# Performance work log

Hardware: AMD Instinct MI355X
Metric: run time of the kernel (lower is better)

The kernel has to match this reference:

```python
import jax, jax.numpy as jnp
import numpy as np

B, L, D_MODEL = 2, 2048, 1024
N_HEADS, D_K = 16, 64  # d_v == d_k (required by the output*q epilogue)


def setup_inputs() -> dict:
    key = jax.random.key(0)
    ks = jax.random.split(key, 8)
    # xavier_normal std for [d_model, d_k] fan: sqrt(2/(d_model+d_k))
    std = float(np.sqrt(2.0 / (D_MODEL + D_K)))
    std_p = float(np.sqrt(1.0 / (N_HEADS * D_K)))  # nn.Linear default ~ U(-1/sqrt(fan_in),..); normal approx ok for a baseline
    return {
        "q": jax.random.normal(ks[0], (B, L, D_MODEL), jnp.float32),
        "k": jax.random.normal(ks[1], (B, L, D_MODEL), jnp.float32),
        "v": jax.random.normal(ks[2], (B, L, D_MODEL), jnp.float32),
        "w_qs": jax.random.normal(ks[3], (N_HEADS, D_MODEL, D_K), jnp.float32) * std,
        "w_ks": jax.random.normal(ks[4], (N_HEADS, D_MODEL, D_K), jnp.float32) * std,
        "w_vs": jax.random.normal(ks[5], (N_HEADS, D_MODEL, D_K), jnp.float32) * std,
        "w_proj": jax.random.normal(ks[6], (D_MODEL, N_HEADS * D_K), jnp.float32) * std_p,
        "b_proj": jnp.zeros((D_MODEL,), jnp.float32),
    }


def reference(q, k, v, w_qs, w_ks, w_vs, w_proj, b_proj):
    # Per-head projections: [h, B, L, d_k]
    qh = jnp.einsum("bld,hdk->hblk", q, w_qs)
    kh = jnp.einsum("bld,hdk->hblk", k, w_ks)
    vh = jnp.einsum("bld,hdk->hblk", v, w_vs)
    # UNscaled attention (no 1/sqrt(d_k)), dropout is identity at eval
    attn = jax.nn.softmax(jnp.einsum("hblk,hbmk->hblm", qh, kh), axis=-1)
    # attn @ V with elementwise *q epilogue
    out = jnp.einsum("hblm,hbmk->hblk", attn, vh) * qh
    # torch.cat(torch.split(outputs, mb_size, 0), -1): heads concat on last dim
    out = out.transpose(1, 2, 0, 3).reshape(q.shape[0], q.shape[1], -1)  # [B, L, h*d_k]
    return out @ w_proj.T + b_proj
```

## Files before the change

kernel.cpp:

```cpp
#include <hip/hip_runtime.h>

#define B_ 2
#define L_ 2048
#define DM 1024
#define H_ 16
#define DK 64
#define ROWS (B_*L_)
#define BK 32
#define LDT 40

typedef _Float16 f16x8 __attribute__((ext_vector_type(8)));
typedef float    f32x4 __attribute__((ext_vector_type(4)));
typedef unsigned short us8 __attribute__((ext_vector_type(8)));
typedef unsigned short us4v __attribute__((ext_vector_type(4)));

__device__ __forceinline__ unsigned short f2h(float f) {
    _Float16 h = (_Float16)f;
    return __builtin_bit_cast(unsigned short, h);
}
__device__ __forceinline__ float h2f(unsigned short u) {
    return (float)__builtin_bit_cast(_Float16, u);
}
__device__ __forceinline__ f16x8 ld8h(const unsigned short* p) {
    return *reinterpret_cast<const f16x8*>(p);
}
__device__ __forceinline__ us8 cvt_us8(float4 a, float4 b) {
    us8 u;
    u[0] = f2h(a.x); u[1] = f2h(a.y); u[2] = f2h(a.z); u[3] = f2h(a.w);
    u[4] = f2h(b.x); u[5] = f2h(b.y); u[6] = f2h(b.z); u[7] = f2h(b.w);
    return u;
}

#define MFMA(a, b, c) __builtin_amdgcn_mfma_f32_16x16x32_f16((a), (b), (c), 0, 0, 0)

#define AS1 __attribute__((address_space(1)))
#define AS3 __attribute__((address_space(3)))
__device__ __forceinline__ void glds16(const void* g, void* l) {
    __builtin_amdgcn_global_load_lds((const AS1 unsigned int*)g,
                                     (AS3 unsigned int*)l, 16, 0, 0);
}

__global__ __launch_bounds__(256) void kcvt(
    const float* __restrict__ src, unsigned short* __restrict__ dst)
{
    size_t i = ((size_t)blockIdx.x * 256 + threadIdx.x) * 8;
    const float4* s4 = (const float4*)(src + i);
    *(us8*)(dst + i) = cvt_us8(s4[0], s4[1]);
}

__global__ __launch_bounds__(256) void kcvt3(
    const float* __restrict__ q, const float* __restrict__ k,
    const float* __restrict__ v, unsigned short* __restrict__ dst)
{
    int bx = blockIdx.x;
    int which = bx >> 11, rem = bx & 2047;
    const float* src = (which == 0) ? q : (which == 1) ? k : v;
    size_t i = ((size_t)rem * 256 + threadIdx.x) * 8;
    const float4* s4 = (const float4*)(src + i);
    *(us8*)(dst + (size_t)which * ROWS * DM + i) = cvt_us8(s4[0], s4[1]);
}

__global__ __launch_bounds__(256) void k0_transpose_w(
    const float* __restrict__ wq,
    const float* __restrict__ wk,
    const float* __restrict__ wv,
    unsigned short* __restrict__ wt)
{
    __shared__ unsigned short tile[64][65];
    int bx = blockIdx.x;
    int which = bx / (H_ * 16);
    int rem   = bx % (H_ * 16);
    int h  = rem >> 4;
    int db = (rem & 15) * 64;
    const float* src = (which == 0) ? wq : (which == 1) ? wk : wv;
    float scale = (which == 1) ? 1.44269504f : 1.0f;

    int t = threadIdx.x;
    int r = t >> 2;
    int c = (t & 3) * 16;
    const float4* sp = (const float4*)(src + ((size_t)(h * DM + db + r)) * DK + c);
    #pragma unroll
    for (int i4 = 0; i4 < 4; i4++) {
        float4 f = sp[i4];
        tile[r][c + i4 * 4 + 0] = f2h(f.x * scale);
        tile[r][c + i4 * 4 + 1] = f2h(f.y * scale);
        tile[r][c + i4 * 4 + 2] = f2h(f.z * scale);
        tile[r][c + i4 * 4 + 3] = f2h(f.w * scale);
    }
    __syncthreads();

    int n   = t >> 2;
    int d16 = (t & 3) * 16;
    __align__(16) unsigned short ov[16];
    #pragma unroll
    for (int i = 0; i < 16; i++) ov[i] = tile[d16 + i][n];
    size_t off = (((size_t)which * H_ + h) * DK + n) * DM + db + d16;
    *(us8*)(wt + off)     = *(us8*)&ov[0];
    *(us8*)(wt + off + 8) = *(us8*)&ov[8];
}

__global__ __launch_bounds__(256) void k1_proj_fp16(
    const unsigned short* __restrict__ qkvh,
    const unsigned short* __restrict__ wt,
    unsigned short* __restrict__ qh,
    unsigned short* __restrict__ kh,
    unsigned short* __restrict__ vt)
{
    __shared__ __align__(16) unsigned short sA[128 * BK];
    __shared__ __align__(16) unsigned short sB[128 * BK];

    int bx = blockIdx.x;
    int which = bx >> 8;
    int rem   = bx & 255;
    int mbase = (rem >> 3) * 128;
    int nbase = (rem & 7) * 128;

    const unsigned short* Ag = qkvh + (size_t)which * ROWS * DM;
    const unsigned short* Bg = wt + (size_t)which * DM * DM;

    int t = threadIdx.x;
    int wave = t >> 6, lane = t & 63, quad = lane >> 4, l16 = lane & 15;
    int wm = (wave >> 1) * 64, wn = (wave & 1) * 64;

    const unsigned short* gA0 = Ag + (size_t)(mbase + (t >> 2)) * DM + (t & 3) * 8;
    const unsigned short* gA1 = gA0 + (size_t)64 * DM;
    const unsigned short* gB0 = Bg + (size_t)(nbase + (t >> 2)) * DM + (t & 3) * 8;
    const unsigned short* gB1 = gB0 + (size_t)64 * DM;
    unsigned short* lA0 = &sA[(size_t)t * 8];
    unsigned short* lA1 = &sA[(size_t)(256 + t) * 8];
    unsigned short* lB0 = &sB[(size_t)t * 8];
    unsigned short* lB1 = &sB[(size_t)(256 + t) * 8];

    f32x4 acc[4][4];
    #pragma unroll
    for (int mi = 0; mi < 4; mi++)
        #pragma unroll
        for (int ni = 0; ni < 4; ni++) acc[mi][ni] = (f32x4)0.0f;

    for (int step = 0; step < 32; step++) {
        if (step) __syncthreads();
        glds16(gA0, lA0); glds16(gA1, lA1);
        glds16(gB0, lB0); glds16(gB1, lB1);
        gA0 += BK; gA1 += BK; gB0 += BK; gB1 += BK;
        __syncthreads();

        f16x8 aF[4], bF[4];
        #pragma unroll
        for (int mi = 0; mi < 4; mi++)
            aF[mi] = *(const f16x8*)&sA[(wm + mi * 16 + l16) * BK + quad * 8];
        #pragma unroll
        for (int ni = 0; ni < 4; ni++)
            bF[ni] = *(const f16x8*)&sB[(wn + ni * 16 + l16) * BK + quad * 8];
        __builtin_amdgcn_s_setprio(1);
        #pragma unroll
        for (int mi = 0; mi < 4; mi++)
            #pragma unroll
            for (int ni = 0; ni < 4; ni++)
                acc[mi][ni] = MFMA(aF[mi], bF[ni], acc[mi][ni]);
        __builtin_amdgcn_s_setprio(0);
    }

    int h = (nbase >> 6) + (wave & 1);
    if (which < 2) {
        unsigned short* OUT = ((which == 0) ? qh : kh) + (size_t)h * ROWS * DK;
        #pragma unroll
        for (int mi = 0; mi < 4; mi++)
            #pragma unroll
            for (int ni = 0; ni < 4; ni++)
                #pragma unroll
                for (int r = 0; r < 4; r++) {
                    int row = mbase + wm + mi * 16 + quad * 4 + r;
                    OUT[(size_t)row * DK + ni * 16 + l16] = f2h(acc[mi][ni][r]);
                }
    } else {
        unsigned short* OUT = vt + (size_t)h * DK * ROWS;
        #pragma unroll
        for (int mi = 0; mi < 4; mi++)
            #pragma unroll
            for (int ni = 0; ni < 4; ni++) {
                int dk   = ni * 16 + l16;
                int rowb = mbase + wm + mi * 16 + quad * 4;
                us4v pk;
                pk[0] = f2h(acc[mi][ni][0]); pk[1] = f2h(acc[mi][ni][1]);
                pk[2] = f2h(acc[mi][ni][2]); pk[3] = f2h(acc[mi][ni][3]);
                *(us4v*)(OUT + (size_t)dk * ROWS + rowb) = pk;
            }
    }
}

__global__ __launch_bounds__(256) void k1_proj_qkv(
    const float* __restrict__ q,
    const float* __restrict__ k,
    const float* __restrict__ v,
    const unsigned short* __restrict__ wt,
    unsigned short* __restrict__ qh,
    unsigned short* __restrict__ kh,
    unsigned short* __restrict__ vt)
{
    __shared__ __align__(16) unsigned short sA[128 * LDT];
    __shared__ __align__(16) unsigned short sB[128 * LDT];

    int bx = blockIdx.x;
    int which = bx >> 8;
    int rem   = bx & 255;
    int mbase = (rem >> 3) * 128;
    int nbase = (rem & 7) * 128;

    const float* Ag = (which == 0) ? q : (which == 1) ? k : v;
    const unsigned short* Bg = wt + (size_t)which * DM * DM;

    int t = threadIdx.x;
    int wave = t >> 6, lane = t & 63, quad = lane >> 4, l16 = lane & 15;
    int wm = (wave >> 1) * 64, wn = (wave & 1) * 64;

    int ar0 = t >> 2,         ac0 = t & 3;
    int ar1 = (256 + t) >> 2, ac1 = t & 3;
    const float* pA0 = Ag + (size_t)(mbase + ar0) * DM + ac0 * 8;
    const float* pA1 = Ag + (size_t)(mbase + ar1) * DM + ac1 * 8;
    const unsigned short* pB0 = Bg + (size_t)(nbase + ar0) * DM + ac0 * 8;
    const unsigned short* pB1 = Bg + (size_t)(nbase + ar1) * DM + ac1 * 8;
    unsigned short* wA0 = &sA[ar0 * LDT + ac0 * 8];
    unsigned short* wA1 = &sA[ar1 * LDT + ac1 * 8];
    unsigned short* wB0 = &sB[ar0 * LDT + ac0 * 8];
    unsigned short* wB1 = &sB[ar1 * LDT + ac1 * 8];

    f32x4 acc[4][4];
    #pragma unroll
    for (int mi = 0; mi < 4; mi++)
        #pragma unroll
        for (int ni = 0; ni < 4; ni++) acc[mi][ni] = (f32x4)0.0f;

    float4 rA0a = *(const float4*)pA0, rA0b = *(const float4*)(pA0 + 4);
    float4 rA1a = *(const float4*)pA1, rA1b = *(const float4*)(pA1 + 4);
    us8 rB0 = *(const us8*)pB0, rB1 = *(const us8*)pB1;

    for (int step = 0; step < 32; step++) {
        if (step) __syncthreads();
        *(us8*)wA0 = cvt_us8(rA0a, rA0b);
        *(us8*)wA1 = cvt_us8(rA1a, rA1b);
        *(us8*)wB0 = rB0; *(us8*)wB1 = rB1;
        __syncthreads();
        if (step < 31) {
            pA0 += BK; pA1 += BK; pB0 += BK; pB1 += BK;
            rA0a = *(const float4*)pA0; rA0b = *(const float4*)(pA0 + 4);
            rA1a = *(const float4*)pA1; rA1b = *(const float4*)(pA1 + 4);
            rB0 = *(const us8*)pB0; rB1 = *(const us8*)pB1;
        }
        f16x8 aF[4], bF[4];
        #pragma unroll
        for (int mi = 0; mi < 4; mi++)
            aF[mi] = *(const f16x8*)&sA[(wm + mi * 16 + l16) * LDT + quad * 8];
        #pragma unroll
        for (int ni = 0; ni < 4; ni++)
            bF[ni] = *(const f16x8*)&sB[(wn + ni * 16 + l16) * LDT + quad * 8];
        #pragma unroll
        for (int mi = 0; mi < 4; mi++)
            #pragma unroll
            for (int ni = 0; ni < 4; ni++)
                acc[mi][ni] = MFMA(aF[mi], bF[ni], acc[mi][ni]);
    }

    int h = (nbase >> 6) + (wave & 1);
    if (which < 2) {
        unsigned short* OUT = ((which == 0) ? qh : kh) + (size_t)h * ROWS * DK;
        #pragma unroll
        for (int mi = 0; mi < 4; mi++)
            #pragma unroll
            for (int ni = 0; ni < 4; ni++)
                #pragma unroll
                for (int r = 0; r < 4; r++) {
                    int row = mbase + wm + mi * 16 + quad * 4 + r;
                    OUT[(size_t)row * DK + ni * 16 + l16] = f2h(acc[mi][ni][r]);
                }
    } else {
        unsigned short* OUT = vt + (size_t)h * DK * ROWS;
        #pragma unroll
        for (int mi = 0; mi < 4; mi++)
            #pragma unroll
            for (int ni = 0; ni < 4; ni++) {
                int dk   = ni * 16 + l16;
                int rowb = mbase + wm + mi * 16 + quad * 4;
                us4v pk;
                pk[0] = f2h(acc[mi][ni][0]); pk[1] = f2h(acc[mi][ni][1]);
                pk[2] = f2h(acc[mi][ni][2]); pk[3] = f2h(acc[mi][ni][3]);
                *(us4v*)(OUT + (size_t)dk * ROWS + rowb) = pk;
            }
    }
}

__global__ __launch_bounds__(256) void k2_attn(
    const unsigned short* __restrict__ qh,
    const unsigned short* __restrict__ kh,
    const unsigned short* __restrict__ vt,
    unsigned short* __restrict__ x2)
{
    __shared__ __align__(16) unsigned short ktile[2][64][64];
    __shared__ __align__(16) unsigned short vtile[2][64][64];
    __shared__ __align__(16) unsigned short pld[4][16][64];

    int bx = blockIdx.x;
    int xcd = bx & 7;
    int loc = bx >> 3;
    int hb  = xcd * 4 + (loc >> 5);
    int qt  = loc & 31;
    int h = hb >> 1, b = hb & 1;
    int qbase = qt * 64;

    const unsigned short* qhp = qh + ((size_t)h * ROWS + b * L_) * DK;
    const unsigned short* khp = kh + ((size_t)h * ROWS + b * L_) * DK;
    const unsigned short* vtp = vt + (size_t)h * DK * ROWS + b * L_;

    int wave = threadIdx.x >> 6, lane = threadIdx.x & 63;
    int quad = lane >> 4, l16 = lane & 15;
    int t = threadIdx.x;
    int g8 = (l16 & 7) * 8;

    int c0 = t,       key0 = c0 >> 3, ss0 = ((c0 & 7) ^ (key0 & 7)) * 8;
    int c1 = 256 + t, key1 = c1 >> 3, ss1 = ((c1 & 7) ^ (key1 & 7)) * 8;
    const unsigned short* kg0 = khp + (size_t)key0 * DK + ss0;
    const unsigned short* kg1 = khp + (size_t)key1 * DK + ss1;
    const unsigned short* vg0 = vtp + (size_t)key0 * ROWS + ss0;
    const unsigned short* vg1 = vtp + (size_t)key1 * ROWS + ss1;
    unsigned short* kl0[2] = { &ktile[0][0][0] + c0 * 8, &ktile[1][0][0] + c0 * 8 };
    unsigned short* kl1[2] = { &ktile[0][0][0] + c1 * 8, &ktile[1][0][0] + c1 * 8 };
    unsigned short* vl0[2] = { &vtile[0][0][0] + c0 * 8, &vtile[1][0][0] + c0 * 8 };
    unsigned short* vl1[2] = { &vtile[0][0][0] + c1 * 8, &vtile[1][0][0] + c1 * 8 };

    glds16(kg0, kl0[0]); glds16(kg1, kl1[0]);
    glds16(vg0, vl0[0]); glds16(vg1, vl1[0]);

    int qrow = qbase + wave * 16 + l16;
    f16x8 qb0 = ld8h(qhp + (size_t)qrow * DK + quad * 8);
    f16x8 qb1 = ld8h(qhp + (size_t)qrow * DK + 32 + quad * 8);

    float m_i = -1e30f, l_i = 0.0f;
    f32x4 o[4];
    #pragma unroll
    for (int nt = 0; nt < 4; nt++) o[nt] = (f32x4)0.0f;

    __syncthreads();

    int cur = 0;
    for (int kt = 0; kt < 32; kt++) {
        if (kt < 31) {
            size_t ko = (size_t)(kt + 1) * 64 * DK;
            size_t vo = (size_t)(kt + 1) * 64;
            int nb = cur ^ 1;
            glds16(kg0 + ko, kl0[nb]); glds16(kg1 + ko, kl1[nb]);
            glds16(vg0 + vo, vl0[nb]); glds16(vg1 + vo, vl1[nb]);
        }

        f32x4 s[4];
        #pragma unroll
        for (int nt = 0; nt < 4; nt++) s[nt] = (f32x4)0.0f;
        __builtin_amdgcn_s_setprio(1);
        #pragma unroll
        for (int nt = 0; nt < 4; nt++) {
            const unsigned short* kr = &ktile[cur][nt * 16 + l16][0];
            f16x8 ka0 = *(const f16x8*)(kr + ((quad * 8) ^ g8));
            f16x8 ka1 = *(const f16x8*)(kr + ((32 + quad * 8) ^ g8));
            s[nt] = MFMA(ka0, qb0, s[nt]);
            s[nt] = MFMA(ka1, qb1, s[nt]);
        }
        __builtin_amdgcn_s_setprio(0);

        float pm[4];
        #pragma unroll
        for (int nt = 0; nt < 4; nt++) {
            float a = fmaxf(s[nt][0], s[nt][1]);
            float c2 = fmaxf(s[nt][2], s[nt][3]);
            pm[nt] = fmaxf(a, c2);
        }
        float mx = fmaxf(fmaxf(pm[0], pm[1]), fmaxf(pm[2], pm[3]));
        mx = fmaxf(mx, __shfl_xor(mx, 16));
        mx = fmaxf(mx, __shfl_xor(mx, 32));

        if (!__all(mx - m_i <= 11.0f)) {
            float mnew  = fmaxf(m_i, mx);
            float alpha = __builtin_amdgcn_exp2f(m_i - mnew);
            l_i *= alpha;
            #pragma unroll
            for (int r = 0; r < 4; r++) {
                float av = __shfl(alpha, quad * 4 + r);
                #pragma unroll
                for (int nt = 0; nt < 4; nt++) o[nt][r] *= av;
            }
            m_i = mnew;
        }

        float ps[4];
        #pragma unroll
        for (int nt = 0; nt < 4; nt++) {
            float e0 = __builtin_amdgcn_exp2f(s[nt][0] - m_i);
            float e1 = __builtin_amdgcn_exp2f(s[nt][1] - m_i);
            float e2 = __builtin_amdgcn_exp2f(s[nt][2] - m_i);
            float e3 = __builtin_amdgcn_exp2f(s[nt][3] - m_i);
            s[nt][0] = e0; s[nt][1] = e1; s[nt][2] = e2; s[nt][3] = e3;
            ps[nt] = (e0 + e1) + (e2 + e3);
        }
        float rs = (ps[0] + ps[1]) + (ps[2] + ps[3]);
        rs += __shfl_xor(rs, 16);
        rs += __shfl_xor(rs, 32);
        l_i += rs;

        #pragma unroll
        for (int nt = 0; nt < 4; nt++) {
            us4v pk;
            pk[0] = f2h(s[nt][0]); pk[1] = f2h(s[nt][1]);
            pk[2] = f2h(s[nt][2]); pk[3] = f2h(s[nt][3]);
            *(us4v*)&pld[wave][l16][(nt * 16 + quad * 4) ^ g8] = pk;
        }

        __builtin_amdgcn_s_setprio(1);
        #pragma unroll
        for (int kk = 0; kk < 2; kk++) {
            f16x8 pa = *(const f16x8*)&pld[wave][l16][(kk * 32 + quad * 8) ^ g8];
            #pragma unroll
            for (int nt = 0; nt < 4; nt++) {
                const unsigned short* vr = &vtile[cur][nt * 16 + l16][0];
                f16x8 vb = *(const f16x8*)(vr + ((kk * 32 + quad * 8) ^ g8));
                o[nt] = MFMA(pa, vb, o[nt]);
            }
        }
        __builtin_amdgcn_s_setprio(0);

        __syncthreads();
        cur ^= 1;
    }

    float linv = 1.0f / l_i;
    #pragma unroll
    for (int r = 0; r < 4; r++) {
        float lv = __shfl(linv, quad * 4 + r);
        int row = qbase + wave * 16 + quad * 4 + r;
        #pragma unroll
        for (int nt = 0; nt < 4; nt++) {
            int col = nt * 16 + l16;
            float qv = h2f(qhp[(size_t)row * DK + col]);
            float val = o[nt][r] * lv * qv;
            x2[((size_t)b * L_ + row) * DM + h * DK + col] = f2h(val);
        }
    }
}

__global__ __launch_bounds__(256) void k3_out_proj(
    const unsigned short* __restrict__ x2,
    const unsigned short* __restrict__ wph,
    const float* __restrict__ bias,
    float* __restrict__ out)
{
    __shared__ __align__(16) unsigned short sA[128 * BK];
    __shared__ __align__(16) unsigned short sB[128 * BK];

    int bx = blockIdx.x;
    int mbase = (bx >> 3) * 128;
    int nbase = (bx & 7) * 128;

    int t = threadIdx.x;
    int wave = t >> 6, lane = t & 63, quad = lane >> 4, l16 = lane & 15;
    int wm = (wave >> 1) * 64, wn = (wave & 1) * 64;

    const unsigned short* gA0 = x2 + (size_t)(mbase + (t >> 2)) * DM + (t & 3) * 8;
    const unsigned short* gA1 = gA0 + (size_t)64 * DM;
    const unsigned short* gB0 = wph + (size_t)(nbase + (t >> 2)) * DM + (t & 3) * 8;
    const unsigned short* gB1 = gB0 + (size_t)64 * DM;
    unsigned short* lA0 = &sA[(size_t)t * 8];
    unsigned short* lA1 = &sA[(size_t)(256 + t) * 8];
    unsigned short* lB0 = &sB[(size_t)t * 8];
    unsigned short* lB1 = &sB[(size_t)(256 + t) * 8];

    f32x4 acc[4][4];
    #pragma unroll
    for (int mi = 0; mi < 4; mi++)
        #pragma unroll
        for (int ni = 0; ni < 4; ni++) acc[mi][ni] = (f32x4)0.0f;

    for (int step = 0; step < 32; step++) {
        if (step) __syncthreads();
        glds16(gA0, lA0); glds16(gA1, lA1);
        glds16(gB0, lB0); glds16(gB1, lB1);
        gA0 += BK; gA1 += BK; gB0 += BK; gB1 += BK;
        __syncthreads();

        f16x8 aF[4], bF[4];
        #pragma unroll
        for (int mi = 0; mi < 4; mi++)
            aF[mi] = *(const f16x8*)&sA[(wm + mi * 16 + l16) * BK + quad * 8];
        #pragma unroll
        for (int ni = 0; ni < 4; ni++)
            bF[ni] = *(const f16x8*)&sB[(wn + ni * 16 + l16) * BK + quad * 8];
        __builtin_amdgcn_s_setprio(1);
        #pragma unroll
        for (int mi = 0; mi < 4; mi++)
            #pragma unroll
            for (int ni = 0; ni < 4; ni++)
                acc[mi][ni] = MFMA(aF[mi], bF[ni], acc[mi][ni]);
        __builtin_amdgcn_s_setprio(0);
    }

    float bv[4];
    #pragma unroll
    for (int ni = 0; ni < 4; ni++) bv[ni] = bias[nbase + wn + ni * 16 + l16];

    #pragma unroll
    for (int mi = 0; mi < 4; mi++)
        #pragma unroll
        for (int ni = 0; ni < 4; ni++)
            #pragma unroll
            for (int r = 0; r < 4; r++) {
                int row = mbase + wm + mi * 16 + quad * 4 + r;
                int col = nbase + wn + ni * 16 + l16;
                out[(size_t)row * DM + col] = acc[mi][ni][r] + bv[ni];
            }
}

extern "C" void kernel_launch(void* const* d_in, const int* in_sizes, int n_in,
                              void* d_out, int out_size, void* d_ws, size_t ws_size,
                              hipStream_t stream)
{
    const float* q     = (const float*)d_in[0];
    const float* k     = (const float*)d_in[1];
    const float* v     = (const float*)d_in[2];
    const float* wqs   = (const float*)d_in[3];
    const float* wks   = (const float*)d_in[4];
    const float* wvs   = (const float*)d_in[5];
    const float* wproj = (const float*)d_in[6];
    const float* bproj = (const float*)d_in[7];
    float* out = (float*)d_out;

    char* ws = (char*)d_ws;
    #define MB (size_t)(1024 * 1024)
    unsigned short* wt   = (unsigned short*)(ws);
    unsigned short* wph  = (unsigned short*)(ws + 6  * MB);
    unsigned short* qh   = (unsigned short*)(ws + 8  * MB);
    unsigned short* kh   = (unsigned short*)(ws + 16 * MB);
    unsigned short* vt   = (unsigned short*)(ws + 24 * MB);
    unsigned short* x2   = (unsigned short*)(ws + 32 * MB);
    unsigned short* qkvh = (unsigned short*)(ws + 32 * MB);

    kcvt<<<dim3((DM * DM) / (256 * 8)), dim3(256), 0, stream>>>(wproj, wph);
    k0_transpose_w<<<dim3(3 * H_ * 16), dim3(256), 0, stream>>>(wqs, wks, wvs, wt);

    if (ws_size >= 56 * MB) {
        kcvt3<<<dim3(3 * 2048), dim3(256), 0, stream>>>(q, k, v, qkvh);
        k1_proj_fp16<<<dim3(3 * 32 * 8), dim3(256), 0, stream>>>(qkvh, wt, qh, kh, vt);
    } else {
        k1_proj_qkv<<<dim3(3 * 32 * 8), dim3(256), 0, stream>>>(q, k, v, wt, qh, kh, vt);
    }
    k2_attn<<<dim3(H_ * B_ * 32), dim3(256), 0, stream>>>(qh, kh, vt, x2);
    k3_out_proj<<<dim3(32 * 8), dim3(256), 0, stream>>>(x2, wph, bproj, out);
}
```

Baseline: 249.1 us.

## Software-pipeline QK^T of next tile with softmax and PV of current tile

```diff
diff --git a/kernel.cpp b/kernel.cpp
--- a/kernel.cpp
+++ b/kernel.cpp
@@ -326,7 +326,13 @@
     unsigned short* vl0[2] = { &vtile[0][0][0] + c0 * 8, &vtile[1][0][0] + c0 * 8 };
     unsigned short* vl1[2] = { &vtile[0][0][0] + c1 * 8, &vtile[1][0][0] + c1 * 8 };
 
+    const unsigned short* kgp0 = kg0 + (size_t)2 * 64 * DK;
+    const unsigned short* kgp1 = kg1 + (size_t)2 * 64 * DK;
+    const unsigned short* vgp0 = vg0 + 64;
+    const unsigned short* vgp1 = vg1 + 64;
+
     glds16(kg0, kl0[0]); glds16(kg1, kl1[0]);
+    glds16(kg0 + (size_t)64 * DK, kl0[1]); glds16(kg1 + (size_t)64 * DK, kl1[1]);
     glds16(vg0, vl0[0]); glds16(vg1, vl1[0]);
 
     int qrow = qbase + wave * 16 + l16;
@@ -338,95 +344,113 @@
     #pragma unroll
     for (int nt = 0; nt < 4; nt++) o[nt] = (f32x4)0.0f;
 
+    f32x4 s0[4], s1[4];
+
     __syncthreads();
 
-    int cur = 0;
-    for (int kt = 0; kt < 32; kt++) {
-        if (kt < 31) {
-            size_t ko = (size_t)(kt + 1) * 64 * DK;
-            size_t vo = (size_t)(kt + 1) * 64;
-            int nb = cur ^ 1;
-            glds16(kg0 + ko, kl0[nb]); glds16(kg1 + ko, kl1[nb]);
-            glds16(vg0 + vo, vl0[nb]); glds16(vg1 + vo, vl1[nb]);
-        }
-
-        f32x4 s[4];
-        #pragma unroll
-        for (int nt = 0; nt < 4; nt++) s[nt] = (f32x4)0.0f;
-        __builtin_amdgcn_s_setprio(1);
-        #pragma unroll
-        for (int nt = 0; nt < 4; nt++) {
-            const unsigned short* kr = &ktile[cur][nt * 16 + l16][0];
-            f16x8 ka0 = *(const f16x8*)(kr + ((quad * 8) ^ g8));
-            f16x8 ka1 = *(const f16x8*)(kr + ((32 + quad * 8) ^ g8));
-            s[nt] = MFMA(ka0, qb0, s[nt]);
-            s[nt] = MFMA(ka1, qb1, s[nt]);
-        }
-        __builtin_amdgcn_s_setprio(0);
-
-        float pm[4];
-        #pragma unroll
-        for (int nt = 0; nt < 4; nt++) {
-            float a = fmaxf(s[nt][0], s[nt][1]);
-            float c2 = fmaxf(s[nt][2], s[nt][3]);
-            pm[nt] = fmaxf(a, c2);
-        }
-        float mx = fmaxf(fmaxf(pm[0], pm[1]), fmaxf(pm[2], pm[3]));
-        mx = fmaxf(mx, __shfl_xor(mx, 16));
-        mx = fmaxf(mx, __shfl_xor(mx, 32));
-
-        if (!__all(mx - m_i <= 11.0f)) {
-            float mnew  = fmaxf(m_i, mx);
-            float alpha = __builtin_amdgcn_exp2f(m_i - mnew);
-            l_i *= alpha;
-            #pragma unroll
-            for (int r = 0; r < 4; r++) {
-                float av = __shfl(alpha, quad * 4 + r);
-                #pragma unroll
-                for (int nt = 0; nt < 4; nt++) o[nt][r] *= av;
-            }
-            m_i = mnew;
-        }
-
-        float ps[4];
-        #pragma unroll
-        for (int nt = 0; nt < 4; nt++) {
-            float e0 = __builtin_amdgcn_exp2f(s[nt][0] - m_i);
-            float e1 = __builtin_amdgcn_exp2f(s[nt][1] - m_i);
-            float e2 = __builtin_amdgcn_exp2f(s[nt][2] - m_i);
-            float e3 = __builtin_amdgcn_exp2f(s[nt][3] - m_i);
-            s[nt][0] = e0; s[nt][1] = e1; s[nt][2] = e2; s[nt][3] = e3;
-            ps[nt] = (e0 + e1) + (e2 + e3);
-        }
-        float rs = (ps[0] + ps[1]) + (ps[2] + ps[3]);
-        rs += __shfl_xor(rs, 16);
-        rs += __shfl_xor(rs, 32);
-        l_i += rs;
-
-        #pragma unroll
-        for (int nt = 0; nt < 4; nt++) {
-            us4v pk;
-            pk[0] = f2h(s[nt][0]); pk[1] = f2h(s[nt][1]);
-            pk[2] = f2h(s[nt][2]); pk[3] = f2h(s[nt][3]);
-            *(us4v*)&pld[wave][l16][(nt * 16 + quad * 4) ^ g8] = pk;
-        }
-
-        __builtin_amdgcn_s_setprio(1);
-        #pragma unroll
-        for (int kk = 0; kk < 2; kk++) {
-            f16x8 pa = *(const f16x8*)&pld[wave][l16][(kk * 32 + quad * 8) ^ g8];
-            #pragma unroll
-            for (int nt = 0; nt < 4; nt++) {
-                const unsigned short* vr = &vtile[cur][nt * 16 + l16][0];
-                f16x8 vb = *(const f16x8*)(vr + ((kk * 32 + quad * 8) ^ g8));
-                o[nt] = MFMA(pa, vb, o[nt]);
-            }
-        }
-        __builtin_amdgcn_s_setprio(0);
-
-        __syncthreads();
-        cur ^= 1;
-    }
+    #pragma unroll
+    for (int nt = 0; nt < 4; nt++) s0[nt] = (f32x4)0.0f;
+    __builtin_amdgcn_s_setprio(1);
+    #pragma unroll
+    for (int nt = 0; nt < 4; nt++) {
+        const unsigned short* kr = &ktile[0][nt * 16 + l16][0];
+        f16x8 ka0 = *(const f16x8*)(kr + ((quad * 8) ^ g8));
+        f16x8 ka1 = *(const f16x8*)(kr + ((32 + quad * 8) ^ g8));
+        s0[nt] = MFMA(ka0, qb0, s0[nt]);
+        s0[nt] = MFMA(ka1, qb1, s0[nt]);
+    }
+    __builtin_amdgcn_s_setprio(0);
+    __syncthreads();
+
+#define K2_BODY(SP, SN, KT, CUR)                                              \
+    {                                                                         \
+        if ((KT) < 31) {                                                      \
+            _Pragma("unroll")                                                 \
+            for (int nt = 0; nt < 4; nt++) SN[nt] = (f32x4)0.0f;              \
+            __builtin_amdgcn_s_setprio(1);                                    \
+            _Pragma("unroll")                                                 \
+            for (int nt = 0; nt < 4; nt++) {                                  \
+                const unsigned short* kr = &ktile[(CUR)^1][nt * 16 + l16][0]; \
+                f16x8 ka0 = *(const f16x8*)(kr + ((quad * 8) ^ g8));          \
+                f16x8 ka1 = *(const f16x8*)(kr + ((32 + quad * 8) ^ g8));     \
+                SN[nt] = MFMA(ka0, qb0, SN[nt]);                              \
+                SN[nt] = MFMA(ka1, qb1, SN[nt]);                              \
+            }                                                                 \
+            __builtin_amdgcn_s_setprio(0);                                    \
+        }                                                                     \
+        if ((KT) < 30) {                                                      \
+            glds16(kgp0, kl0[CUR]); glds16(kgp1, kl1[CUR]);                   \
+            kgp0 += (size_t)64 * DK; kgp1 += (size_t)64 * DK;                 \
+        }                                                                     \
+        if ((KT) < 31) {                                                      \
+            glds16(vgp0, vl0[(CUR)^1]); glds16(vgp1, vl1[(CUR)^1]);           \
+            vgp0 += 64; vgp1 += 64;                                           \
+        }                                                                     \
+                                                 \
+        float pm[4];                                                          \
+        _Pragma("unroll")                                                     \
+        for (int nt = 0; nt < 4; nt++) {                                      \
+            float a = fmaxf(SP[nt][0], SP[nt][1]);                            \
+            float c2 = fmaxf(SP[nt][2], SP[nt][3]);                           \
+            pm[nt] = fmaxf(a, c2);                                            \
+        }                                                                     \
+        float mx = fmaxf(fmaxf(pm[0], pm[1]), fmaxf(pm[2], pm[3]));           \
+        mx = fmaxf(mx, __shfl_xor(mx, 16));                                   \
+        mx = fmaxf(mx, __shfl_xor(mx, 32));                                   \
+        if (!__all(mx - m_i <= 11.0f)) {                                      \
+            float mnew  = fmaxf(m_i, mx);                                     \
+            float alpha = __builtin_amdgcn_exp2f(m_i - mnew);                 \
+            l_i *= alpha;                                                     \
+            _Pragma("unroll")                                                 \
+            for (int r = 0; r < 4; r++) {                                     \
+                float av = __shfl(alpha, quad * 4 + r);                       \
+                _Pragma("unroll")                                             \
+                for (int nt = 0; nt < 4; nt++) o[nt][r] *= av;                \
+            }                                                                 \
+            m_i = mnew;                                                       \
+        }                                                                     \
+        float ps[4];                                                          \
+        _Pragma("unroll")                                                     \
+        for (int nt = 0; nt < 4; nt++) {                                      \
+            float e0 = __builtin_amdgcn_exp2f(SP[nt][0] - m_i);               \
+            float e1 = __builtin_amdgcn_exp2f(SP[nt][1] - m_i);               \
+            float e2 = __builtin_amdgcn_exp2f(SP[nt][2] - m_i);               \
+            float e3 = __builtin_amdgcn_exp2f(SP[nt][3] - m_i);               \
+            SP[nt][0] = e0; SP[nt][1] = e1; SP[nt][2] = e2; SP[nt][3] = e3;   \
+            ps[nt] = (e0 + e1) + (e2 + e3);                                   \
+        }                                                                     \
+        float rs = (ps[0] + ps[1]) + (ps[2] + ps[3]);                         \
+        rs += __shfl_xor(rs, 16);                                             \
+        rs += __shfl_xor(rs, 32);                                             \
+        l_i += rs;                                                            \
+        _Pragma("unroll")                                                     \
+        for (int nt = 0; nt < 4; nt++) {                                      \
+            us4v pk;                                                          \
+            pk[0] = f2h(SP[nt][0]); pk[1] = f2h(SP[nt][1]);                   \
+            pk[2] = f2h(SP[nt][2]); pk[3] = f2h(SP[nt][3]);                   \
+            *(us4v*)&pld[wave][l16][(nt * 16 + quad * 4) ^ g8] = pk;          \
+        }                                                                     \
+                                                      \
+        __builtin_amdgcn_s_setprio(1);                                        \
+        _Pragma("unroll")                                                     \
+        for (int kk = 0; kk < 2; kk++) {                                      \
+            f16x8 pa = *(const f16x8*)&pld[wave][l16][(kk*32 + quad*8) ^ g8]; \
+            _Pragma("unroll")                                                 \
+            for (int nt = 0; nt < 4; nt++) {                                  \
+                const unsigned short* vr = &vtile[CUR][nt * 16 + l16][0];     \
+                f16x8 vb = *(const f16x8*)(vr + ((kk * 32 + quad * 8) ^ g8)); \
+                o[nt] = MFMA(pa, vb, o[nt]);                                  \
+            }                                                                 \
+        }                                                                     \
+        __builtin_amdgcn_s_setprio(0);                                        \
+        __syncthreads();                                                      \
+    }
+
+    for (int kt = 0; kt < 32; kt += 2) {
+        K2_BODY(s0, s1, kt,     0)
+        K2_BODY(s1, s0, kt + 1, 1)
+    }
+#undef K2_BODY
 
     float linv = 1.0f / l_i;
     #pragma unroll
```

Result: slower. 254.8 us (+2.3%).

## Remap blocks for XCD locality, load weights via direct-to-LDS, raise MFMA priority

Applied to the files above, without the earlier changes.

```diff
diff --git a/kernel.cpp b/kernel.cpp
--- a/kernel.cpp
+++ b/kernel.cpp
@@ -109,7 +109,8 @@
     __shared__ __align__(16) unsigned short sA[128 * BK];
     __shared__ __align__(16) unsigned short sB[128 * BK];
 
-    int bx = blockIdx.x;
+    int bxr = blockIdx.x;
+    int bx  = (bxr & 7) * 96 + (bxr >> 3);
     int which = bx >> 8;
     int rem   = bx & 255;
     int mbase = (rem >> 3) * 128;
@@ -198,9 +199,10 @@
     unsigned short* __restrict__ vt)
 {
     __shared__ __align__(16) unsigned short sA[128 * LDT];
-    __shared__ __align__(16) unsigned short sB[128 * LDT];
-
-    int bx = blockIdx.x;
+    __shared__ __align__(16) unsigned short sB[128 * BK];
+
+    int bxr = blockIdx.x;
+    int bx  = (bxr & 7) * 96 + (bxr >> 3);
     int which = bx >> 8;
     int rem   = bx & 255;
     int mbase = (rem >> 3) * 128;
@@ -217,12 +219,12 @@
     int ar1 = (256 + t) >> 2, ac1 = t & 3;
     const float* pA0 = Ag + (size_t)(mbase + ar0) * DM + ac0 * 8;
     const float* pA1 = Ag + (size_t)(mbase + ar1) * DM + ac1 * 8;
-    const unsigned short* pB0 = Bg + (size_t)(nbase + ar0) * DM + ac0 * 8;
-    const unsigned short* pB1 = Bg + (size_t)(nbase + ar1) * DM + ac1 * 8;
+    const unsigned short* gB0 = Bg + (size_t)(nbase + (t >> 2)) * DM + (t & 3) * 8;
+    const unsigned short* gB1 = gB0 + (size_t)64 * DM;
     unsigned short* wA0 = &sA[ar0 * LDT + ac0 * 8];
     unsigned short* wA1 = &sA[ar1 * LDT + ac1 * 8];
-    unsigned short* wB0 = &sB[ar0 * LDT + ac0 * 8];
-    unsigned short* wB1 = &sB[ar1 * LDT + ac1 * 8];
+    unsigned short* lB0 = &sB[(size_t)t * 8];
+    unsigned short* lB1 = &sB[(size_t)(256 + t) * 8];
 
     f32x4 acc[4][4];
     #pragma unroll
@@ -232,19 +234,18 @@
 
     float4 rA0a = *(const float4*)pA0, rA0b = *(const float4*)(pA0 + 4);
     float4 rA1a = *(const float4*)pA1, rA1b = *(const float4*)(pA1 + 4);
-    us8 rB0 = *(const us8*)pB0, rB1 = *(const us8*)pB1;
 
     for (int step = 0; step < 32; step++) {
         if (step) __syncthreads();
         *(us8*)wA0 = cvt_us8(rA0a, rA0b);
         *(us8*)wA1 = cvt_us8(rA1a, rA1b);
-        *(us8*)wB0 = rB0; *(us8*)wB1 = rB1;
+        glds16(gB0, lB0); glds16(gB1, lB1);
+        gB0 += BK; gB1 += BK;
         __syncthreads();
         if (step < 31) {
-            pA0 += BK; pA1 += BK; pB0 += BK; pB1 += BK;
+            pA0 += BK; pA1 += BK;
             rA0a = *(const float4*)pA0; rA0b = *(const float4*)(pA0 + 4);
             rA1a = *(const float4*)pA1; rA1b = *(const float4*)(pA1 + 4);
-            rB0 = *(const us8*)pB0; rB1 = *(const us8*)pB1;
         }
         f16x8 aF[4], bF[4];
         #pragma unroll
@@ -252,12 +253,14 @@
             aF[mi] = *(const f16x8*)&sA[(wm + mi * 16 + l16) * LDT + quad * 8];
         #pragma unroll
         for (int ni = 0; ni < 4; ni++)
-            bF[ni] = *(const f16x8*)&sB[(wn + ni * 16 + l16) * LDT + quad * 8];
+            bF[ni] = *(const f16x8*)&sB[(wn + ni * 16 + l16) * BK + quad * 8];
+        __builtin_amdgcn_s_setprio(1);
         #pragma unroll
         for (int mi = 0; mi < 4; mi++)
             #pragma unroll
             for (int ni = 0; ni < 4; ni++)
                 acc[mi][ni] = MFMA(aF[mi], bF[ni], acc[mi][ni]);
+        __builtin_amdgcn_s_setprio(0);
     }
 
     int h = (nbase >> 6) + (wave & 1);
@@ -452,7 +455,8 @@
     __shared__ __align__(16) unsigned short sA[128 * BK];
     __shared__ __align__(16) unsigned short sB[128 * BK];
 
-    int bx = blockIdx.x;
+    int bxr = blockIdx.x;
+    int bx  = (bxr & 7) * 32 + (bxr >> 3);
     int mbase = (bx >> 3) * 128;
     int nbase = (bx & 7) * 128;
 
```

Measured after the change: 241.1 us. -3.2%, faster.
